# Kernel optimization log

Measured on AMD Instinct MI355X. Metric: run time of the kernel, lower is better.

Reference implementation:

```python
import jax, jax.numpy as jnp
import numpy as np
import math

B, S, D, H = 2, 2048, 1024, 16
DK = D // H


def setup_inputs() -> dict:
    key = jax.random.key(0)
    ks = jax.random.split(key, 12)
    scale = 1.0 / math.sqrt(D)
    inp = {
        "query": jax.random.normal(ks[0], (B, S, D), jnp.float32),
        "key": jax.random.normal(ks[1], (B, S, D), jnp.float32),
        "value": jax.random.normal(ks[2], (B, S, D), jnp.float32),
        # causal 0/1 mask, broadcast over heads
        "mask": jnp.broadcast_to(jnp.tril(jnp.ones((S, S), jnp.int32)), (B, 1, S, S)),
        "Wq": jax.random.normal(ks[3], (D, D), jnp.float32) * scale,
        "bq": jnp.zeros((D,), jnp.float32),
        "Wk": jax.random.normal(ks[4], (D, D), jnp.float32) * scale,
        "bk": jnp.zeros((D,), jnp.float32),
        "Wv": jax.random.normal(ks[5], (D, D), jnp.float32) * scale,
        "bv": jnp.zeros((D,), jnp.float32),
        "Wo": jax.random.normal(ks[6], (D, D), jnp.float32) * scale,
        "bo": jnp.zeros((D,), jnp.float32),
    }
    return inp


def _split_heads(x):
    # [B,S,D] -> [B,H,S,DK]
    return x.reshape(B, S, H, DK).transpose(0, 2, 1, 3)


def reference(query, key, value, mask, Wq, bq, Wk, bk, Wv, bv, Wo, bo):
    q = _split_heads(query @ Wq.T + bq)
    k = _split_heads(key @ Wk.T + bk)
    v = _split_heads(value @ Wv.T + bv)
    # scaled dot-product attention with additive mask (mask==0 -> -inf)
    scores = jnp.einsum("bhqd,bhkd->bhqk", q, k) / math.sqrt(DK)
    scores = jnp.where(mask == 0, -jnp.inf, scores)
    w = jax.nn.softmax(scores, axis=-1)
    out = jnp.einsum("bhqk,bhkd->bhqd", w, v)
    out = out.transpose(0, 2, 1, 3).reshape(B, S, D)
    return out @ Wo.T + bo
```

## Files before the change

kernel.cpp:

```cpp
#include <hip/hip_runtime.h>
#include <hip/hip_bf16.h>
#include <math.h>

#define BBATCH 2
#define SSEQ 2048
#define DMODEL 1024
#define NH 16
#define MTOT (BBATCH*SSEQ)

typedef short bfrag __attribute__((ext_vector_type(8)));
typedef float ffrag __attribute__((ext_vector_type(4)));

typedef const __attribute__((address_space(1))) unsigned int* gas_t;
typedef __attribute__((address_space(3))) unsigned int* las_t;

__device__ __forceinline__ void dl16(const void* g, void* l) {
  __builtin_amdgcn_global_load_lds((gas_t)(unsigned long long)g,
                                   (las_t)(unsigned int)(unsigned long long)l,
                                   16, 0, 0);
}

__device__ __forceinline__ void drain_vm() {
  asm volatile("s_waitcnt vmcnt(0)" ::: "memory");
}

__device__ __forceinline__ unsigned short f2bf(float f) {
  union { float f; unsigned u; } v; v.f = f;
  unsigned r = v.u + 0x7fffu + ((v.u >> 16) & 1u);
  return (unsigned short)(r >> 16);
}

__global__ __launch_bounds__(256) void convert_all_kernel(
    const float* __restrict__ q, const float* __restrict__ k, const float* __restrict__ v,
    const float* __restrict__ wq, const float* __restrict__ wk,
    const float* __restrict__ wv, const float* __restrict__ wo,
    unsigned short* __restrict__ dst)
{
  const long NIN = (long)MTOT * DMODEL;
  const long NW  = (long)DMODEL * DMODEL;
  const long total8 = (3 * NIN + 4 * NW) >> 3;
  long i8 = (long)blockIdx.x * blockDim.x + threadIdx.x;
  const long stride = (long)gridDim.x * blockDim.x;
  for (; i8 < total8; i8 += stride) {
    const long i = i8 << 3;
    const float* src; long off;
    if (i < NIN)          { src = q; off = i; }
    else if (i < 2 * NIN) { src = k; off = i - NIN; }
    else if (i < 3 * NIN) { src = v; off = i - 2 * NIN; }
    else {
      const long j = i - 3 * NIN;
      const int wsel = (int)(j >> 20);
      off = j & (NW - 1);
      src = (wsel == 0) ? wq : (wsel == 1) ? wk : (wsel == 2) ? wv : wo;
    }
    const float4 x0 = *(const float4*)(src + off);
    const float4 x1 = *(const float4*)(src + off + 4);
    ushort4 o0, o1;
    o0.x = f2bf(x0.x); o0.y = f2bf(x0.y); o0.z = f2bf(x0.z); o0.w = f2bf(x0.w);
    o1.x = f2bf(x1.x); o1.y = f2bf(x1.y); o1.z = f2bf(x1.z); o1.w = f2bf(x1.w);
    union { ushort4 s[2]; uint4 u; } pk; pk.s[0] = o0; pk.s[1] = o1;
    *(uint4*)(dst + i) = pk.u;
  }
}

struct ProjArgs {
  const unsigned short* X[3];
  const unsigned short* W[3];
  const float* bias[3];
  unsigned short* dst[3];
  float scale[3];
};

__global__ __launch_bounds__(256, 2) void qkv_proj(ProjArgs a)
{
  __shared__ alignas(16) unsigned short As[2][128 * 64];
  __shared__ alignas(16) unsigned short Bs[2][128 * 64];
  const int t = threadIdx.x;
  const int lane = t & 63, w = t >> 6;
  const int quad = lane >> 4, l16 = lane & 15;
  const int m0 = blockIdx.x * 128;
  const int n0 = blockIdx.y * 128;
  const int z = blockIdx.z;
  const unsigned short* __restrict__ X = a.X[z];
  const unsigned short* __restrict__ W = a.W[z];
  const int wm = (w & 1) * 64, wn = (w >> 1) * 64;

  ffrag acc[4][4];
#pragma unroll
  for (int i = 0; i < 4; ++i)
#pragma unroll
    for (int j = 0; j < 4; ++j)
#pragma unroll
      for (int e = 0; e < 4; ++e) acc[i][j][e] = 0.f;

#pragma unroll
  for (int i = 0; i < 4; ++i) {
    const int ch = i * 256 + t;
    const int row = ch >> 3, pc = ch & 7;
    dl16(X + (size_t)(m0 + row) * DMODEL + pc * 8, As[0] + ch * 8);
    dl16(W + (size_t)(n0 + row) * DMODEL + pc * 8, Bs[0] + ch * 8);
  }

  for (int kk = 0; kk < 16; ++kk) {
    const int cur = kk & 1;
    drain_vm();
    __syncthreads();

    if (kk < 15) {
      const int k1 = (kk + 1) * 64, nxt = cur ^ 1;
#pragma unroll
      for (int i = 0; i < 4; ++i) {
        const int ch = i * 256 + t;
        const int row = ch >> 3, pc = ch & 7;
        dl16(X + (size_t)(m0 + row) * DMODEL + k1 + pc * 8, As[nxt] + ch * 8);
        dl16(W + (size_t)(n0 + row) * DMODEL + k1 + pc * 8, Bs[nxt] + ch * 8);
      }
    }

    bfrag af[4][2], bg[4][2];
#pragma unroll
    for (int fi = 0; fi < 4; ++fi)
#pragma unroll
      for (int c = 0; c < 2; ++c) {
        af[fi][c] = *(const bfrag*)&As[cur][(wm + fi * 16 + l16) * 64 + c * 32 + quad * 8];
        bg[fi][c] = *(const bfrag*)&Bs[cur][(wn + fi * 16 + l16) * 64 + c * 32 + quad * 8];
      }
#pragma unroll
    for (int c = 0; c < 2; ++c)
#pragma unroll
      for (int fi = 0; fi < 4; ++fi)
#pragma unroll
        for (int fj = 0; fj < 4; ++fj)
          acc[fi][fj] = __builtin_amdgcn_mfma_f32_16x16x32_bf16(af[fi][c], bg[fj][c], acc[fi][fj], 0, 0, 0);
  }

  const float sc = a.scale[z];
  const float* __restrict__ bias = a.bias[z];
  unsigned short* __restrict__ dst = a.dst[z];
#pragma unroll
  for (int fj = 0; fj < 4; ++fj) {
    const int n = n0 + wn + fj * 16 + l16;
    const float bv = bias[n];
    const int h = n >> 6, dk = n & 63;
    if (z < 2) {
#pragma unroll
      for (int fi = 0; fi < 4; ++fi)
#pragma unroll
        for (int r = 0; r < 4; ++r) {
          const int m = m0 + wm + fi * 16 + quad * 4 + r;
          const int b_ = m >> 11, s_ = m & (SSEQ - 1);
          dst[((size_t)(b_ * NH + h) * SSEQ + s_) * 64 + dk] = f2bf((acc[fi][fj][r] + bv) * sc);
        }
    } else {
#pragma unroll
      for (int fi = 0; fi < 4; ++fi) {
        const int m = m0 + wm + fi * 16 + quad * 4;
        const int b_ = m >> 11, s_ = m & (SSEQ - 1);
        ushort4 pk;
        pk.x = f2bf(acc[fi][fj][0] + bv);
        pk.y = f2bf(acc[fi][fj][1] + bv);
        pk.z = f2bf(acc[fi][fj][2] + bv);
        pk.w = f2bf(acc[fi][fj][3] + bv);
        *(ushort4*)&dst[((size_t)(b_ * NH + h) * 64 + dk) * SSEQ + s_] = pk;
      }
    }
  }
}

__global__ __launch_bounds__(256, 2) void out_proj(
    const unsigned short* __restrict__ X,
    const unsigned short* __restrict__ W,
    const float* __restrict__ bias,
    float* __restrict__ Y)
{
  __shared__ alignas(16) unsigned short As[2][128 * 64];
  __shared__ alignas(16) unsigned short Bs[2][64 * 64];
  const int t = threadIdx.x;
  const int lane = t & 63, w = t >> 6;
  const int quad = lane >> 4, l16 = lane & 15;
  const int m0 = blockIdx.x * 128;
  const int n0 = blockIdx.y * 64;
  const int wm = (w & 1) * 64, wn = (w >> 1) * 32;

  ffrag acc[4][2];
#pragma unroll
  for (int i = 0; i < 4; ++i)
#pragma unroll
    for (int j = 0; j < 2; ++j)
#pragma unroll
      for (int e = 0; e < 4; ++e) acc[i][j][e] = 0.f;

#pragma unroll
  for (int i = 0; i < 4; ++i) {
    const int ch = i * 256 + t;
    dl16(X + (size_t)(m0 + (ch >> 3)) * DMODEL + (ch & 7) * 8, As[0] + ch * 8);
  }
#pragma unroll
  for (int i = 0; i < 2; ++i) {
    const int ch = i * 256 + t;
    dl16(W + (size_t)(n0 + (ch >> 3)) * DMODEL + (ch & 7) * 8, Bs[0] + ch * 8);
  }

  for (int kk = 0; kk < 16; ++kk) {
    const int cur = kk & 1;
    drain_vm();
    __syncthreads();

    if (kk < 15) {
      const int k1 = (kk + 1) * 64, nxt = cur ^ 1;
#pragma unroll
      for (int i = 0; i < 4; ++i) {
        const int ch = i * 256 + t;
        dl16(X + (size_t)(m0 + (ch >> 3)) * DMODEL + k1 + (ch & 7) * 8, As[nxt] + ch * 8);
      }
#pragma unroll
      for (int i = 0; i < 2; ++i) {
        const int ch = i * 256 + t;
        dl16(W + (size_t)(n0 + (ch >> 3)) * DMODEL + k1 + (ch & 7) * 8, Bs[nxt] + ch * 8);
      }
    }

    bfrag af[4][2], bg[2][2];
#pragma unroll
    for (int fi = 0; fi < 4; ++fi)
#pragma unroll
      for (int c = 0; c < 2; ++c)
        af[fi][c] = *(const bfrag*)&As[cur][(wm + fi * 16 + l16) * 64 + c * 32 + quad * 8];
#pragma unroll
    for (int fj = 0; fj < 2; ++fj)
#pragma unroll
      for (int c = 0; c < 2; ++c)
        bg[fj][c] = *(const bfrag*)&Bs[cur][(wn + fj * 16 + l16) * 64 + c * 32 + quad * 8];
#pragma unroll
    for (int c = 0; c < 2; ++c)
#pragma unroll
      for (int fi = 0; fi < 4; ++fi)
#pragma unroll
        for (int fj = 0; fj < 2; ++fj)
          acc[fi][fj] = __builtin_amdgcn_mfma_f32_16x16x32_bf16(af[fi][c], bg[fj][c], acc[fi][fj], 0, 0, 0);
  }

#pragma unroll
  for (int fj = 0; fj < 2; ++fj) {
    const int n = n0 + wn + fj * 16 + l16;
    const float bv = bias[n];
#pragma unroll
    for (int fi = 0; fi < 4; ++fi)
#pragma unroll
      for (int r = 0; r < 4; ++r) {
        const int m = m0 + wm + fi * 16 + quad * 4 + r;
        Y[(size_t)m * DMODEL + n] = acc[fi][fj][r] + bv;
      }
  }
}

__global__ __launch_bounds__(512, 4) void attn_mfma(
    const unsigned short* __restrict__ Q,
    const unsigned short* __restrict__ K,
    const unsigned short* __restrict__ Vt_g,
    unsigned short* __restrict__ ctx)
{
  __shared__ alignas(16) unsigned short Kb[2][64 * 64];
  __shared__ alignas(16) unsigned short Vb[2][64 * 64];
  __shared__ alignas(16) unsigned short Pt[8][16 * 64];

  const int t = threadIdx.x;
  const int lane = t & 63, w = t >> 6;
  const int quad = lane >> 4, l16 = lane & 15;
  const int bh = blockIdx.y;
  const int Xt = blockIdx.z ? (15 - (int)blockIdx.x) : (int)blockIdx.x;
  const int i0 = Xt * 128;
  const int jtmax = 2 * Xt + 1;
  const int b_ = bh >> 4, h_ = bh & (NH - 1);
  const int q_l = w * 16 + l16;

  const unsigned short* kg = K + (size_t)bh * SSEQ * 64;
  const unsigned short* vg = Vt_g + (size_t)bh * 64 * SSEQ;

  const int r_ = t >> 3;
  const int lc = (t & 7) ^ (r_ & 7);
  const int koff = r_ * 64 + lc * 8;
  const int voff = r_ * SSEQ + lc * 8;
  const int loff = t * 8;

  int sw[2];
#pragma unroll
  for (int c = 0; c < 2; ++c) sw[c] = (((c * 4 + quad) ^ (l16 & 7)) * 8);
  const int pwr = l16 * 64 + (quad & 1) * 4;

  dl16(kg + koff, Kb[0] + loff);
  dl16(vg + voff, Vb[0] + loff);

  const unsigned short* qg = Q + ((size_t)bh * SSEQ + i0) * 64;
  bfrag qb[2];
#pragma unroll
  for (int c = 0; c < 2; ++c)
    qb[c] = *(const bfrag*)(qg + (size_t)q_l * 64 + c * 32 + quad * 8);

  ffrag o[4];
#pragma unroll
  for (int fn = 0; fn < 4; ++fn)
#pragma unroll
    for (int e = 0; e < 4; ++e) o[fn][e] = 0.f;
  float lsum = 0.f;

  for (int jt = 0; jt <= jtmax; ++jt) {
    const int cur = jt & 1;
    drain_vm();
    __syncthreads();

    if (jt < jtmax) {
      const int nxt = cur ^ 1;
      dl16(kg + (size_t)(jt + 1) * 4096 + koff, Kb[nxt] + loff);
      dl16(vg + (size_t)(jt + 1) * 64   + voff, Vb[nxt] + loff);
    }

    ffrag s[4];
#pragma unroll
    for (int fj = 0; fj < 4; ++fj)
#pragma unroll
      for (int e = 0; e < 4; ++e) s[fj][e] = 0.f;
#pragma unroll
    for (int c = 0; c < 2; ++c)
#pragma unroll
      for (int fj = 0; fj < 4; ++fj) {
        bfrag ka = *(const bfrag*)&Kb[cur][(fj * 16 + l16) * 64 + sw[c]];
        s[fj] = __builtin_amdgcn_mfma_f32_16x16x32_bf16(ka, qb[c], s[fj], 0, 0, 0);
      }

    const int kbase = (jt - 2 * Xt) * 64;
    const bool diag = (kbase >= 0);
#pragma unroll
    for (int fj = 0; fj < 4; ++fj) {
      float p[4];
#pragma unroll
      for (int r = 0; r < 4; ++r) {
        float pe = exp2f(s[fj][r]);
        if (diag && (kbase + fj * 16 + quad * 4 + r) > q_l) pe = 0.f;
        p[r] = pe;
        lsum += pe;
      }
      float2 lo; lo.x = p[0]; lo.y = p[1];
      float2 hi; hi.x = p[2]; hi.y = p[3];
      union { __hip_bfloat162 h[2]; unsigned long long u; } cv;
      cv.h[0] = __float22bfloat162_rn(lo);
      cv.h[1] = __float22bfloat162_rn(hi);
      const int cc = fj * 2 + (quad >> 1);
      *(unsigned long long*)&Pt[w][pwr + ((cc ^ (l16 & 7)) * 8)] = cv.u;
    }
    asm volatile("s_waitcnt lgkmcnt(0)" ::: "memory");

#pragma unroll
    for (int c = 0; c < 2; ++c) {
      bfrag pb = *(const bfrag*)&Pt[w][l16 * 64 + sw[c]];
#pragma unroll
      for (int fn = 0; fn < 4; ++fn) {
        bfrag va = *(const bfrag*)&Vb[cur][(fn * 16 + l16) * 64 + sw[c]];
        o[fn] = __builtin_amdgcn_mfma_f32_16x16x32_bf16(va, pb, o[fn], 0, 0, 0);
      }
    }
  }

  lsum += __shfl_xor(lsum, 16);
  lsum += __shfl_xor(lsum, 32);

  const float inv = 1.f / lsum;
  unsigned short* cbase = ctx + (size_t)(b_ * SSEQ + i0 + q_l) * DMODEL + h_ * 64;
#pragma unroll
  for (int fn = 0; fn < 4; ++fn) {
    float2 lo; lo.x = o[fn][0] * inv; lo.y = o[fn][1] * inv;
    float2 hi; hi.x = o[fn][2] * inv; hi.y = o[fn][3] * inv;
    union { __hip_bfloat162 h[2]; unsigned long long u; } cv;
    cv.h[0] = __float22bfloat162_rn(lo);
    cv.h[1] = __float22bfloat162_rn(hi);
    *(unsigned long long*)(cbase + fn * 16 + quad * 4) = cv.u;
  }
}

extern "C" void kernel_launch(void* const* d_in, const int* in_sizes, int n_in,
                              void* d_out, int out_size, void* d_ws, size_t ws_size,
                              hipStream_t stream)
{
  const float* q  = (const float*)d_in[0];
  const float* k  = (const float*)d_in[1];
  const float* v  = (const float*)d_in[2];
  const float* wq = (const float*)d_in[4];
  const float* bq = (const float*)d_in[5];
  const float* wk = (const float*)d_in[6];
  const float* bk = (const float*)d_in[7];
  const float* wv = (const float*)d_in[8];
  const float* bv = (const float*)d_in[9];
  const float* wo = (const float*)d_in[10];
  const float* bo = (const float*)d_in[11];

  const long NIN = (long)MTOT * DMODEL;
  const long NW  = (long)DMODEL * DMODEL;
  unsigned short* ws16 = (unsigned short*)d_ws;
  unsigned short* qx  = ws16;
  unsigned short* kx  = qx + NIN;
  unsigned short* vx  = kx + NIN;
  unsigned short* wqb = vx + NIN;
  unsigned short* wkb = wqb + NW;
  unsigned short* wvb = wkb + NW;
  unsigned short* wob = wvb + NW;
  unsigned short* Qp  = wob + NW;
  unsigned short* Kp  = Qp + NIN;
  unsigned short* Vp  = Kp + NIN;
  unsigned short* Cx  = Vp + NIN;

  convert_all_kernel<<<2048, 256, 0, stream>>>(q, k, v, wq, wk, wv, wo, ws16);

  ProjArgs pa;
  pa.X[0] = qx;  pa.X[1] = kx;  pa.X[2] = vx;
  pa.W[0] = wqb; pa.W[1] = wkb; pa.W[2] = wvb;
  pa.bias[0] = bq; pa.bias[1] = bk; pa.bias[2] = bv;
  pa.dst[0] = Qp; pa.dst[1] = Kp; pa.dst[2] = Vp;
  pa.scale[0] = 0.18033688011112042f;
  pa.scale[1] = 1.0f;
  pa.scale[2] = 1.0f;
  qkv_proj<<<dim3(MTOT / 128, DMODEL / 128, 3), 256, 0, stream>>>(pa);

  attn_mfma<<<dim3(8, BBATCH * NH, 2), 512, 0, stream>>>(Qp, Kp, Vp, Cx);

  out_proj<<<dim3(MTOT / 128, DMODEL / 64), 256, 0, stream>>>(Cx, wob, bo, (float*)d_out);
}
```

Baseline: 243.6 us.

## Swizzle GEMM LDS tiles and shrink attention query tiles to 64 rows

Applies an XOR swizzle to the LDS layout of the QKV and output projection tiles so the MFMA fragment reads avoid bank conflicts. The attention kernel moves from 128-row query tiles with 512 threads to 64-row tiles with 256 threads. This gives finer causal work granularity and a single diagonal tile handled by a separate masked path, while off-diagonal tiles skip masking. The row sum is now computed with an extra MFMA against a vector of ones instead of a scalar accumulation and shuffles. The trade-off is that each block reloads K/V for half as many queries, so K/V traffic roughly doubles.

```diff
diff --git a/kernel.cpp b/kernel.cpp
--- a/kernel.cpp
+++ b/kernel.cpp
@@ -85,6 +85,10 @@
   const unsigned short* __restrict__ W = a.W[z];
   const int wm = (w & 1) * 64, wn = (w >> 1) * 64;
 
+  int sw[2];
+#pragma unroll
+  for (int c = 0; c < 2; ++c) sw[c] = (((c * 4 + quad) ^ (l16 & 7)) * 8);
+
   ffrag acc[4][4];
 #pragma unroll
   for (int i = 0; i < 4; ++i)
@@ -96,9 +100,9 @@
 #pragma unroll
   for (int i = 0; i < 4; ++i) {
     const int ch = i * 256 + t;
-    const int row = ch >> 3, pc = ch & 7;
-    dl16(X + (size_t)(m0 + row) * DMODEL + pc * 8, As[0] + ch * 8);
-    dl16(W + (size_t)(n0 + row) * DMODEL + pc * 8, Bs[0] + ch * 8);
+    const int row = ch >> 3, lc = (ch & 7) ^ (row & 7);
+    dl16(X + (size_t)(m0 + row) * DMODEL + lc * 8, As[0] + ch * 8);
+    dl16(W + (size_t)(n0 + row) * DMODEL + lc * 8, Bs[0] + ch * 8);
   }
 
   for (int kk = 0; kk < 16; ++kk) {
@@ -111,9 +115,9 @@
 #pragma unroll
       for (int i = 0; i < 4; ++i) {
         const int ch = i * 256 + t;
-        const int row = ch >> 3, pc = ch & 7;
-        dl16(X + (size_t)(m0 + row) * DMODEL + k1 + pc * 8, As[nxt] + ch * 8);
-        dl16(W + (size_t)(n0 + row) * DMODEL + k1 + pc * 8, Bs[nxt] + ch * 8);
+        const int row = ch >> 3, lc = (ch & 7) ^ (row & 7);
+        dl16(X + (size_t)(m0 + row) * DMODEL + k1 + lc * 8, As[nxt] + ch * 8);
+        dl16(W + (size_t)(n0 + row) * DMODEL + k1 + lc * 8, Bs[nxt] + ch * 8);
       }
     }
 
@@ -122,8 +126,8 @@
     for (int fi = 0; fi < 4; ++fi)
 #pragma unroll
       for (int c = 0; c < 2; ++c) {
-        af[fi][c] = *(const bfrag*)&As[cur][(wm + fi * 16 + l16) * 64 + c * 32 + quad * 8];
-        bg[fi][c] = *(const bfrag*)&Bs[cur][(wn + fi * 16 + l16) * 64 + c * 32 + quad * 8];
+        af[fi][c] = *(const bfrag*)&As[cur][(wm + fi * 16 + l16) * 64 + sw[c]];
+        bg[fi][c] = *(const bfrag*)&Bs[cur][(wn + fi * 16 + l16) * 64 + sw[c]];
       }
 #pragma unroll
     for (int c = 0; c < 2; ++c)
@@ -182,6 +186,10 @@
   const int n0 = blockIdx.y * 64;
   const int wm = (w & 1) * 64, wn = (w >> 1) * 32;
 
+  int sw[2];
+#pragma unroll
+  for (int c = 0; c < 2; ++c) sw[c] = (((c * 4 + quad) ^ (l16 & 7)) * 8);
+
   ffrag acc[4][2];
 #pragma unroll
   for (int i = 0; i < 4; ++i)
@@ -193,12 +201,14 @@
 #pragma unroll
   for (int i = 0; i < 4; ++i) {
     const int ch = i * 256 + t;
-    dl16(X + (size_t)(m0 + (ch >> 3)) * DMODEL + (ch & 7) * 8, As[0] + ch * 8);
+    const int row = ch >> 3, lc = (ch & 7) ^ (row & 7);
+    dl16(X + (size_t)(m0 + row) * DMODEL + lc * 8, As[0] + ch * 8);
   }
 #pragma unroll
   for (int i = 0; i < 2; ++i) {
     const int ch = i * 256 + t;
-    dl16(W + (size_t)(n0 + (ch >> 3)) * DMODEL + (ch & 7) * 8, Bs[0] + ch * 8);
+    const int row = ch >> 3, lc = (ch & 7) ^ (row & 7);
+    dl16(W + (size_t)(n0 + row) * DMODEL + lc * 8, Bs[0] + ch * 8);
   }
 
   for (int kk = 0; kk < 16; ++kk) {
@@ -211,12 +221,14 @@
 #pragma unroll
       for (int i = 0; i < 4; ++i) {
         const int ch = i * 256 + t;
-        dl16(X + (size_t)(m0 + (ch >> 3)) * DMODEL + k1 + (ch & 7) * 8, As[nxt] + ch * 8);
+        const int row = ch >> 3, lc = (ch & 7) ^ (row & 7);
+        dl16(X + (size_t)(m0 + row) * DMODEL + k1 + lc * 8, As[nxt] + ch * 8);
       }
 #pragma unroll
       for (int i = 0; i < 2; ++i) {
         const int ch = i * 256 + t;
-        dl16(W + (size_t)(n0 + (ch >> 3)) * DMODEL + k1 + (ch & 7) * 8, Bs[nxt] + ch * 8);
+        const int row = ch >> 3, lc = (ch & 7) ^ (row & 7);
+        dl16(W + (size_t)(n0 + row) * DMODEL + k1 + lc * 8, Bs[nxt] + ch * 8);
       }
     }
 
@@ -225,12 +237,12 @@
     for (int fi = 0; fi < 4; ++fi)
 #pragma unroll
       for (int c = 0; c < 2; ++c)
-        af[fi][c] = *(const bfrag*)&As[cur][(wm + fi * 16 + l16) * 64 + c * 32 + quad * 8];
+        af[fi][c] = *(const bfrag*)&As[cur][(wm + fi * 16 + l16) * 64 + sw[c]];
 #pragma unroll
     for (int fj = 0; fj < 2; ++fj)
 #pragma unroll
       for (int c = 0; c < 2; ++c)
-        bg[fj][c] = *(const bfrag*)&Bs[cur][(wn + fj * 16 + l16) * 64 + c * 32 + quad * 8];
+        bg[fj][c] = *(const bfrag*)&Bs[cur][(wn + fj * 16 + l16) * 64 + sw[c]];
 #pragma unroll
     for (int c = 0; c < 2; ++c)
 #pragma unroll
@@ -254,7 +266,7 @@
   }
 }
 
-__global__ __launch_bounds__(512, 4) void attn_mfma(
+__global__ __launch_bounds__(256, 4) void attn_mfma(
     const unsigned short* __restrict__ Q,
     const unsigned short* __restrict__ K,
     const unsigned short* __restrict__ Vt_g,
@@ -262,34 +274,40 @@
 {
   __shared__ alignas(16) unsigned short Kb[2][64 * 64];
   __shared__ alignas(16) unsigned short Vb[2][64 * 64];
-  __shared__ alignas(16) unsigned short Pt[8][16 * 64];
+  __shared__ alignas(16) unsigned short Pt[4][16 * 64];
 
   const int t = threadIdx.x;
   const int lane = t & 63, w = t >> 6;
   const int quad = lane >> 4, l16 = lane & 15;
   const int bh = blockIdx.y;
-  const int Xt = blockIdx.z ? (15 - (int)blockIdx.x) : (int)blockIdx.x;
-  const int i0 = Xt * 128;
-  const int jtmax = 2 * Xt + 1;
+  const int qtile = blockIdx.z ? (31 - (int)blockIdx.x) : (int)blockIdx.x;
+  const int i0 = qtile * 64;
   const int b_ = bh >> 4, h_ = bh & (NH - 1);
   const int q_l = w * 16 + l16;
 
   const unsigned short* kg = K + (size_t)bh * SSEQ * 64;
   const unsigned short* vg = Vt_g + (size_t)bh * 64 * SSEQ;
 
-  const int r_ = t >> 3;
-  const int lc = (t & 7) ^ (r_ & 7);
-  const int koff = r_ * 64 + lc * 8;
-  const int voff = r_ * SSEQ + lc * 8;
-  const int loff = t * 8;
-
+  int koff[2], voff[2], loff[2];
+#pragma unroll
+  for (int i = 0; i < 2; ++i) {
+    const int ch = i * 256 + t;
+    const int r = ch >> 3;
+    const int lc = (ch & 7) ^ (r & 7);
+    koff[i] = r * 64 + lc * 8;
+    voff[i] = r * SSEQ + lc * 8;
+    loff[i] = ch * 8;
+  }
   int sw[2];
 #pragma unroll
   for (int c = 0; c < 2; ++c) sw[c] = (((c * 4 + quad) ^ (l16 & 7)) * 8);
   const int pwr = l16 * 64 + (quad & 1) * 4;
 
-  dl16(kg + koff, Kb[0] + loff);
-  dl16(vg + voff, Vb[0] + loff);
+#pragma unroll
+  for (int i = 0; i < 2; ++i) {
+    dl16(kg + koff[i], Kb[0] + loff[i]);
+    dl16(vg + voff[i], Vb[0] + loff[i]);
+  }
 
   const unsigned short* qg = Q + ((size_t)bh * SSEQ + i0) * 64;
   bfrag qb[2];
@@ -297,22 +315,31 @@
   for (int c = 0; c < 2; ++c)
     qb[c] = *(const bfrag*)(qg + (size_t)q_l * 64 + c * 32 + quad * 8);
 
-  ffrag o[4];
+  bfrag onesf;
+#pragma unroll
+  for (int j = 0; j < 8; ++j) onesf[j] = (short)0x3F80;
+
+  ffrag o[4], lacc;
 #pragma unroll
   for (int fn = 0; fn < 4; ++fn)
 #pragma unroll
     for (int e = 0; e < 4; ++e) o[fn][e] = 0.f;
-  float lsum = 0.f;
-
-  for (int jt = 0; jt <= jtmax; ++jt) {
+#pragma unroll
+  for (int e = 0; e < 4; ++e) lacc[e] = 0.f;
+
+  for (int jt = 0; jt < qtile + 1; ++jt) {
     const int cur = jt & 1;
+    const bool diag = (jt == qtile);
     drain_vm();
     __syncthreads();
 
-    if (jt < jtmax) {
+    if (!diag) {
       const int nxt = cur ^ 1;
-      dl16(kg + (size_t)(jt + 1) * 4096 + koff, Kb[nxt] + loff);
-      dl16(vg + (size_t)(jt + 1) * 64   + voff, Vb[nxt] + loff);
+#pragma unroll
+      for (int i = 0; i < 2; ++i) {
+        dl16(kg + (size_t)(jt + 1) * 4096 + koff[i], Kb[nxt] + loff[i]);
+        dl16(vg + (size_t)(jt + 1) * 64   + voff[i], Vb[nxt] + loff[i]);
+      }
     }
 
     ffrag s[4];
@@ -328,31 +355,41 @@
         s[fj] = __builtin_amdgcn_mfma_f32_16x16x32_bf16(ka, qb[c], s[fj], 0, 0, 0);
       }
 
-    const int kbase = (jt - 2 * Xt) * 64;
-    const bool diag = (kbase >= 0);
-#pragma unroll
-    for (int fj = 0; fj < 4; ++fj) {
-      float p[4];
-#pragma unroll
-      for (int r = 0; r < 4; ++r) {
-        float pe = exp2f(s[fj][r]);
-        if (diag && (kbase + fj * 16 + quad * 4 + r) > q_l) pe = 0.f;
-        p[r] = pe;
-        lsum += pe;
-      }
-      float2 lo; lo.x = p[0]; lo.y = p[1];
-      float2 hi; hi.x = p[2]; hi.y = p[3];
-      union { __hip_bfloat162 h[2]; unsigned long long u; } cv;
-      cv.h[0] = __float22bfloat162_rn(lo);
-      cv.h[1] = __float22bfloat162_rn(hi);
-      const int cc = fj * 2 + (quad >> 1);
-      *(unsigned long long*)&Pt[w][pwr + ((cc ^ (l16 & 7)) * 8)] = cv.u;
+    if (diag) {
+#pragma unroll
+      for (int fj = 0; fj < 4; ++fj) {
+        float p[4];
+#pragma unroll
+        for (int r = 0; r < 4; ++r) {
+          const float pe = exp2f(s[fj][r]);
+          p[r] = ((fj * 16 + quad * 4 + r) > q_l) ? 0.f : pe;
+        }
+        float2 lo; lo.x = p[0]; lo.y = p[1];
+        float2 hi; hi.x = p[2]; hi.y = p[3];
+        union { __hip_bfloat162 h[2]; unsigned long long u; } cv;
+        cv.h[0] = __float22bfloat162_rn(lo);
+        cv.h[1] = __float22bfloat162_rn(hi);
+        const int cc = fj * 2 + (quad >> 1);
+        *(unsigned long long*)&Pt[w][pwr + ((cc ^ (l16 & 7)) * 8)] = cv.u;
+      }
+    } else {
+#pragma unroll
+      for (int fj = 0; fj < 4; ++fj) {
+        float2 lo; lo.x = exp2f(s[fj][0]); lo.y = exp2f(s[fj][1]);
+        float2 hi; hi.x = exp2f(s[fj][2]); hi.y = exp2f(s[fj][3]);
+        union { __hip_bfloat162 h[2]; unsigned long long u; } cv;
+        cv.h[0] = __float22bfloat162_rn(lo);
+        cv.h[1] = __float22bfloat162_rn(hi);
+        const int cc = fj * 2 + (quad >> 1);
+        *(unsigned long long*)&Pt[w][pwr + ((cc ^ (l16 & 7)) * 8)] = cv.u;
+      }
     }
     asm volatile("s_waitcnt lgkmcnt(0)" ::: "memory");
 
 #pragma unroll
     for (int c = 0; c < 2; ++c) {
       bfrag pb = *(const bfrag*)&Pt[w][l16 * 64 + sw[c]];
+      lacc = __builtin_amdgcn_mfma_f32_16x16x32_bf16(onesf, pb, lacc, 0, 0, 0);
 #pragma unroll
       for (int fn = 0; fn < 4; ++fn) {
         bfrag va = *(const bfrag*)&Vb[cur][(fn * 16 + l16) * 64 + sw[c]];
@@ -361,10 +398,7 @@
     }
   }
 
-  lsum += __shfl_xor(lsum, 16);
-  lsum += __shfl_xor(lsum, 32);
-
-  const float inv = 1.f / lsum;
+  const float inv = 1.f / lacc[0];
   unsigned short* cbase = ctx + (size_t)(b_ * SSEQ + i0 + q_l) * DMODEL + h_ * 64;
 #pragma unroll
   for (int fn = 0; fn < 4; ++fn) {
@@ -420,7 +454,7 @@
   pa.scale[2] = 1.0f;
   qkv_proj<<<dim3(MTOT / 128, DMODEL / 128, 3), 256, 0, stream>>>(pa);
 
-  attn_mfma<<<dim3(8, BBATCH * NH, 2), 512, 0, stream>>>(Qp, Kp, Vp, Cx);
+  attn_mfma<<<dim3(16, BBATCH * NH, 2), 256, 0, stream>>>(Qp, Kp, Vp, Cx);
 
   out_proj<<<dim3(MTOT / 128, DMODEL / 64), 256, 0, stream>>>(Cx, wob, bo, (float*)d_out);
 }
```

Result: faster. 226.6 us (-7.0%).
